# Optimization experiments

Measured on AMD Instinct MI355X. Metric: run time of the kernel, lower is better.

The kernel has to match this reference:

```python
import jax, jax.numpy as jnp
import numpy as np

B, M, D = 16384, 40, 32
INPUT_DIM = M * D  # 1280
CIN_SIZES = [128, 128]
DEEP_DIMS = [256, 128, 64]
EPS = 1e-5


def _init_linear(key, fan_in, fan_out):
    k1, k2 = jax.random.split(key)
    bound = 1.0 / np.sqrt(fan_in)
    w = jax.random.uniform(k1, (fan_out, fan_in), jnp.float32, -bound, bound)
    b = jax.random.uniform(k2, (fan_out,), jnp.float32, -bound, bound)
    return w, b


def setup_inputs() -> dict:
    key = jax.random.key(0)
    ks = jax.random.split(key, 12)
    x = jax.random.normal(ks[0], (B, INPUT_DIM), jnp.float32)
    emb_3d = jax.random.normal(ks[1], (B, M, D), jnp.float32)
    lin_w, lin_b = _init_linear(ks[2], INPUT_DIM, 1)
    # CIN conv1d (kernel_size=1) weights, flattened to [out, in]
    conv_w0, conv_b0 = _init_linear(ks[3], M * M, CIN_SIZES[0])          # in = 40*40
    prev1 = CIN_SIZES[0] // 2                                             # split_half
    conv_w1, conv_b1 = _init_linear(ks[4], M * prev1, CIN_SIZES[1])       # in = 40*64
    cin_out_dim = CIN_SIZES[0] // 2 + CIN_SIZES[1]                        # 192
    cin_out_w, cin_out_b = _init_linear(ks[5], cin_out_dim, 1)
    dims = [INPUT_DIM] + DEEP_DIMS
    deep_w0, deep_b0 = _init_linear(ks[6], dims[0], dims[1])
    deep_w1, deep_b1 = _init_linear(ks[7], dims[1], dims[2])
    deep_w2, deep_b2 = _init_linear(ks[8], dims[2], dims[3])
    ln_g0, ln_b0 = jnp.ones((dims[1],), jnp.float32), jnp.zeros((dims[1],), jnp.float32)
    ln_g1, ln_b1 = jnp.ones((dims[2],), jnp.float32), jnp.zeros((dims[2],), jnp.float32)
    ln_g2, ln_b2 = jnp.ones((dims[3],), jnp.float32), jnp.zeros((dims[3],), jnp.float32)
    return dict(x=x, emb_3d=emb_3d, lin_w=lin_w, lin_b=lin_b,
                conv_w0=conv_w0, conv_b0=conv_b0, conv_w1=conv_w1, conv_b1=conv_b1,
                cin_out_w=cin_out_w, cin_out_b=cin_out_b,
                deep_w0=deep_w0, deep_b0=deep_b0, ln_g0=ln_g0, ln_b0=ln_b0,
                deep_w1=deep_w1, deep_b1=deep_b1, ln_g1=ln_g1, ln_b1=ln_b1,
                deep_w2=deep_w2, deep_b2=deep_b2, ln_g2=ln_g2, ln_b2=ln_b2)


def _layernorm(h, g, b):
    mu = jnp.mean(h, axis=-1, keepdims=True)
    var = jnp.mean(jnp.square(h - mu), axis=-1, keepdims=True)
    return (h - mu) * jax.lax.rsqrt(var + EPS) * g + b


def _cin_layer(x0, xi, w, b):
    # outer = einsum('bmd,bnd->bmnd') then 1x1 conv over flattened (m*n).
    # Fused: contract the (m,n) outer product directly with the conv weight.
    o = w.shape[0]
    m, n = x0.shape[1], xi.shape[1]
    w3 = w.reshape(o, m, n)
    out = jnp.einsum('bmd,bnd,omn->bod', x0, xi, w3) + b[None, :, None]
    return jax.nn.relu(out)


def reference(x, emb_3d, lin_w, lin_b,
              conv_w0, conv_b0, conv_w1, conv_b1, cin_out_w, cin_out_b,
              deep_w0, deep_b0, ln_g0, ln_b0,
              deep_w1, deep_b1, ln_g1, ln_b1,
              deep_w2, deep_b2, ln_g2, ln_b2):
    aux = (x @ lin_w.T + lin_b)[:, 0]  # [B]

    # CIN with split_half=True
    x0 = emb_3d                                   # [B, 40, 32]
    out0 = _cin_layer(x0, x0, conv_w0, conv_b0)    # [B, 128, 32]
    h1, direct0 = jnp.split(out0, 2, axis=1)       # hidden gets FIRST half
    out1 = _cin_layer(x0, h1, conv_w1, conv_b1)    # [B, 128, 32]
    cin_feat = jnp.sum(jnp.concatenate([direct0, out1], axis=1), axis=2)  # [B, 192]
    aux = aux + (cin_feat @ cin_out_w.T + cin_out_b)[:, 0]

    # Deep tower (dropout = identity in eval)
    h = jax.nn.relu(_layernorm(x @ deep_w0.T + deep_b0, ln_g0, ln_b0))
    h = jax.nn.relu(_layernorm(h @ deep_w1.T + deep_b1, ln_g1, ln_b1))
    h = jax.nn.relu(_layernorm(h @ deep_w2.T + deep_b2, ln_g2, ln_b2))
    return h, aux
```

## Files before the change

### kernel.cpp

```cpp
#include <hip/hip_runtime.h>
#include <hip/hip_bf16.h>

typedef unsigned int u32;
typedef __attribute__((ext_vector_type(8))) short short8;
typedef __attribute__((ext_vector_type(8))) _Float16 half8;
typedef __attribute__((ext_vector_type(4))) float f32x4;

__device__ __forceinline__ u32 bf16_rne(float f) {
  u32 u = __builtin_bit_cast(u32, f);
  return (u + 0x7fffu + ((u >> 16) & 1u)) >> 16;
}
__device__ __forceinline__ u32 pk_bf16(float a, float b) {
  union { __hip_bfloat162 h; u32 u; } cv;
  cv.h = __float22bfloat162_rn(make_float2(a, b));
  return cv.u;
}
__device__ __forceinline__ unsigned short f16b(float f) {
  return __builtin_bit_cast(unsigned short, (_Float16)f);
}
__device__ __forceinline__ half8 splat8(_Float16 x) {
  return (half8){x, x, x, x, x, x, x, x};
}

__device__ __forceinline__ void glds16(const u32* g, u32* l) {
  __builtin_amdgcn_global_load_lds((const __attribute__((address_space(1))) u32*)g,
                                   (__attribute__((address_space(3))) u32*)l, 16, 0, 0);
}

__global__ void swz_kernel(const float* __restrict__ W, unsigned short* __restrict__ out,
                           int N, int K) {
  int tid = blockIdx.x * 256 + threadIdx.x;
  if (tid >= N * K) return;
  int j = tid & 7, l = (tid >> 3) & 63, rest = tid >> 9;
  int nt = N >> 4;
  int t = rest % nt, k32 = rest / nt;
  int o = t * 16 + (l & 15);
  int k = k32 * 32 + (l >> 4) * 8 + j;
  out[tid] = (unsigned short)bf16_rne(W[(size_t)o * K + k]);
}
__global__ void swz_f16_kernel(const float* __restrict__ W, unsigned short* __restrict__ out,
                               int N, int K) {
  int tid = blockIdx.x * 256 + threadIdx.x;
  if (tid >= N * K) return;
  int j = tid & 7, l = (tid >> 3) & 63, rest = tid >> 9;
  int nt = N >> 4;
  int t = rest % nt, k32 = rest / nt;
  int o = t * 16 + (l & 15);
  int k = k32 * 32 + (l >> 4) * 8 + j;
  out[tid] = f16b(W[(size_t)o * K + k]);
}

__global__ void tbl_kernel(u32* __restrict__ tbl0) {
  int g = threadIdx.x;
  if (g >= 120) return;
  int base = 0, m = 0;
  for (m = 0; m < 40; ++m) {
    int cnt = 5 - (m >> 3);
    if (g < base + cnt) break;
    base += cnt;
  }
  int n0 = 8 * ((m >> 3) + (g - base));
  tbl0[g] = (u32)m | ((u32)n0 << 8);
}

__global__ void swz0s_kernel(const float* __restrict__ W, const u32* __restrict__ tbl0,
                             unsigned short* __restrict__ out) {
  int tid = blockIdx.x * 256 + threadIdx.x;
  if (tid >= 960 * 128) return;
  int j = tid & 7, l = (tid >> 3) & 63, rest = tid >> 9;
  int t = rest & 7, k32 = rest >> 3;
  int o = t * 16 + (l & 15);
  int g = k32 * 4 + (l >> 4);
  u32 te = tbl0[g];
  int m = (int)(te & 255u), n0 = (int)(te >> 8);
  int n = n0 + j;
  float val;
  if (n < m) val = 0.f;
  else if (n == m) val = W[o * 1600 + m * 41];
  else val = W[o * 1600 + m * 40 + n] + W[o * 1600 + n * 40 + m];
  out[tid] = f16b(val);
}

__global__ void lin_kernel(const float* __restrict__ x, const float* __restrict__ lw,
                           const float* __restrict__ lb, const float* __restrict__ cb,
                           float* __restrict__ aux) {
  int row = blockIdx.x * 4 + (threadIdx.x >> 6);
  int lane = threadIdx.x & 63;
  const float4* xr = (const float4*)(x + (size_t)row * 1280);
  const float4* lw4 = (const float4*)lw;
  float s = 0.f;
#pragma unroll
  for (int e = 0; e < 5; ++e) {
    float4 a = xr[e * 64 + lane];
    float4 b = lw4[e * 64 + lane];
    s += a.x * b.x + a.y * b.y + a.z * b.z + a.w * b.w;
  }
#pragma unroll
  for (int m = 1; m < 64; m <<= 1) s += __shfl_xor(s, m, 64);
  if (lane == 0) aux[row] = s + lb[0] + cb[0];
}

__global__ __launch_bounds__(256, 2) void cin_kernel(
    const float* __restrict__ emb, const unsigned short* __restrict__ wz0s,
    const unsigned short* __restrict__ wz1, const u32* __restrict__ tbl0,
    const float* __restrict__ b0v, const float* __restrict__ b1v,
    const float* __restrict__ cw, float* __restrict__ aux) {
  __shared__ __align__(16) unsigned short Xh[128 * 40];
  __shared__ __align__(16) unsigned short h1s[128 * 72];
  __shared__ u32 tbl[120];
  __shared__ float auxacc[128];

  const int tid = threadIdx.x;
  const int lane = tid & 63;
  const int w = tid >> 6;
  const int wr = w >> 1, wc = w & 1;
  const int rl = lane & 15, q = lane >> 4;
  const int b0blk = blockIdx.x * 4;

#pragma unroll
  for (int i = 0; i < 5; ++i) {
    int idx = i * 256 + tid;
    int b = idx / 320;
    int rem = idx - b * 320;
    int m = rem >> 3, d0 = (rem & 7) * 4;
    float4 v = *(const float4*)(emb + ((size_t)(b0blk + b) * 40 + m) * 32 + d0);
    unsigned short* xc = &Xh[(b * 32 + d0) * 40 + m];
    xc[0] = f16b(v.x); xc[40] = f16b(v.y); xc[80] = f16b(v.z); xc[120] = f16b(v.w);
  }
  if (tid < 128) auxacc[tid] = 0.f;
  if (tid < 120) tbl[tid] = tbl0[tid];
  __syncthreads();

  f32x4 acc[4][4];
#pragma unroll
  for (int u = 0; u < 4; ++u)
#pragma unroll
    for (int t = 0; t < 4; ++t) acc[u][t] = f32x4{0.f, 0.f, 0.f, 0.f};

  {
    const u32* bptr = (const u32*)wz0s + wc * 1024 + lane * 4;
    const u32* xw = (const u32*)Xh;
    uint4 bA[4], bB[4];
    uint4 vnA[4], vnB[4];
    _Float16 xmA[4], xmB[4];

    auto loadB0 = [&](int kc, uint4* b) {
#pragma unroll
      for (int tt = 0; tt < 4; ++tt) b[tt] = *(const uint4*)(bptr + kc * 2048 + tt * 256);
    };
    auto loadA0 = [&](int kc, uint4* vn, _Float16* xm) {
      u32 te = tbl[kc * 4 + q];
      int mm = (int)(te & 255u);
      int w0 = (int)(te >> 8) >> 1;
#pragma unroll
      for (int u = 0; u < 4; ++u) {
        int r = 64 * wr + 16 * u + rl;
        vn[u] = *(const uint4*)(xw + r * 20 + w0);
        xm[u] = __builtin_bit_cast(_Float16, Xh[r * 40 + mm]);
      }
    };
    auto mfma0 = [&](const uint4* vn, const _Float16* xm, const uint4* bv) {
      __builtin_amdgcn_s_setprio(1);
#pragma unroll
      for (int u = 0; u < 4; ++u) {
        half8 af = __builtin_bit_cast(half8, vn[u]) * splat8(xm[u]);
#pragma unroll
        for (int tt = 0; tt < 4; ++tt)
          acc[u][tt] = __builtin_amdgcn_mfma_f32_16x16x32_f16(
              af, __builtin_bit_cast(half8, bv[tt]), acc[u][tt], 0, 0, 0);
      }
      __builtin_amdgcn_s_setprio(0);
    };

    loadB0(0, bA);
    loadA0(0, vnA, xmA);
    for (int kc = 0; kc < 30; kc += 2) {
      loadB0(kc + 1, bB);
      loadA0(kc + 1, vnB, xmB);
      mfma0(vnA, xmA, bA);
      int kn = (kc + 2 < 30) ? kc + 2 : 0;
      loadB0(kn, bA);
      loadA0(kn, vnA, xmA);
      mfma0(vnB, xmB, bB);
    }
  }

  if (wc == 0) {
#pragma unroll
    for (int u = 0; u < 4; ++u) {
      int r0q = 64 * wr + 16 * u + 4 * q;
#pragma unroll
      for (int tt = 0; tt < 4; ++tt) {
        int o = 16 * tt + rl;
        float bb = b0v[o];
#pragma unroll
        for (int i = 0; i < 4; ++i) {
          float vv = fmaxf(acc[u][tt][i] + bb, 0.f);
          h1s[(r0q + i) * 72 + o] = f16b(vv);
        }
      }
    }
  } else {
#pragma unroll
    for (int u = 0; u < 4; ++u)
#pragma unroll
      for (int i = 0; i < 4; ++i) {
        float sle = 0.f;
#pragma unroll
        for (int tt = 0; tt < 4; ++tt) {
          int o = 64 + 16 * tt + rl;
          sle += fmaxf(acc[u][tt][i] + b0v[o], 0.f) * cw[o - 64];
        }
        sle += __shfl_xor(sle, 1, 16);
        sle += __shfl_xor(sle, 2, 16);
        sle += __shfl_xor(sle, 4, 16);
        sle += __shfl_xor(sle, 8, 16);
        if (rl == 0) atomicAdd(&auxacc[64 * wr + 16 * u + 4 * q + i], sle);
      }
  }
#pragma unroll
  for (int u = 0; u < 4; ++u)
#pragma unroll
    for (int t = 0; t < 4; ++t) acc[u][t] = f32x4{0.f, 0.f, 0.f, 0.f};
  __syncthreads();

  {
    const u32* bptr = (const u32*)wz1 + wc * 1024 + lane * 4;
    const u32* hw = (const u32*)h1s;
    uint4 bA[4], bB[4];
    uint4 hpA[4], hpB[4];
    _Float16 xmA[4], xmB[4];

    auto loadB1 = [&](int kc, uint4* b) {
#pragma unroll
      for (int tt = 0; tt < 4; ++tt) b[tt] = *(const uint4*)(bptr + kc * 2048 + tt * 256);
    };
    auto loadH = [&](int kc, uint4* hp) {
      int wof = ((kc & 1) << 4) + 4 * q;
#pragma unroll
      for (int u = 0; u < 4; ++u) {
        int r = 64 * wr + 16 * u + rl;
        hp[u] = *(const uint4*)(hw + r * 36 + wof);
      }
    };
    auto loadXM = [&](int kp, _Float16* xm) {
#pragma unroll
      for (int u = 0; u < 4; ++u)
        xm[u] = __builtin_bit_cast(_Float16, Xh[(64 * wr + 16 * u + rl) * 40 + kp]);
    };
    auto mfma1 = [&](const uint4* hp, const _Float16* xm, const uint4* bv) {
      __builtin_amdgcn_s_setprio(1);
#pragma unroll
      for (int u = 0; u < 4; ++u) {
        half8 af = __builtin_bit_cast(half8, hp[u]) * splat8(xm[u]);
#pragma unroll
        for (int tt = 0; tt < 4; ++tt)
          acc[u][tt] = __builtin_amdgcn_mfma_f32_16x16x32_f16(
              af, __builtin_bit_cast(half8, bv[tt]), acc[u][tt], 0, 0, 0);
      }
      __builtin_amdgcn_s_setprio(0);
    };

    loadB1(0, bA);
    loadH(0, hpA);
    loadXM(0, xmA);
    for (int kp = 0; kp < 40; ++kp) {
      int kc = 2 * kp;
      loadB1(kc + 1, bB);
      loadH(kc + 1, hpB);
      mfma1(hpA, xmA, bA);
      int kc2 = (kc + 2 < 80) ? kc + 2 : 0;
      int kn = (kp + 1 < 40) ? kp + 1 : 0;
      loadB1(kc2, bA);
      loadH(kc2, hpA);
      loadXM(kn, xmB);
      mfma1(hpB, xmA, bB);
#pragma unroll
      for (int u = 0; u < 4; ++u) xmA[u] = xmB[u];
    }
  }

#pragma unroll
  for (int u = 0; u < 4; ++u)
#pragma unroll
    for (int i = 0; i < 4; ++i) {
      float sle = 0.f;
#pragma unroll
      for (int tt = 0; tt < 4; ++tt) {
        int o = 64 * wc + 16 * tt + rl;
        sle += fmaxf(acc[u][tt][i] + b1v[o], 0.f) * cw[64 + o];
      }
      sle += __shfl_xor(sle, 1, 16);
      sle += __shfl_xor(sle, 2, 16);
      sle += __shfl_xor(sle, 4, 16);
      sle += __shfl_xor(sle, 8, 16);
      if (rl == 0) atomicAdd(&auxacc[64 * wr + 16 * u + 4 * q + i], sle);
    }
  __syncthreads();
  if (tid < 4) {
    float ssum = 0.f;
    for (int d = 0; d < 32; ++d) ssum += auxacc[tid * 32 + d];
    aux[b0blk + tid] += ssum;
  }
}

template <int NT, bool AF32>
__global__ __launch_bounds__(256, 2) void gemm_deep(
    const void* __restrict__ Ain, const unsigned short* __restrict__ Bswz,
    const float* __restrict__ bias, float* __restrict__ Cout, int M, int N, int K) {
  __shared__ unsigned short At[128 * 40];
  __shared__ u32 Bt[NT * 256];
  const int tid = threadIdx.x, lane = tid & 63, w = tid >> 6;
  const int wr = w >> 1, wc = w & 1, rl = lane & 15, q = lane >> 4;
  const int r0 = blockIdx.x * 128, c0 = blockIdx.y * (NT * 16);
  const int ntg = N >> 4;
  constexpr int WT = NT / 2;
  f32x4 acc[4][WT];
#pragma unroll
  for (int u = 0; u < 4; ++u)
#pragma unroll
    for (int t = 0; t < WT; ++t) acc[u][t] = f32x4{0.f, 0.f, 0.f, 0.f};

  for (int kk = 0; kk < K; kk += 32) {
    __syncthreads();
    {
      int r = tid >> 1, kh = (tid & 1) * 16;
      if constexpr (AF32) {
        const float* A = (const float*)Ain;
        const float* src = A + (size_t)(r0 + r) * K + kk + kh;
        float4 v0 = *(const float4*)src;
        float4 v1 = *(const float4*)(src + 4);
        float4 v2 = *(const float4*)(src + 8);
        float4 v3 = *(const float4*)(src + 12);
        uint4 p0, p1;
        p0.x = pk_bf16(v0.x, v0.y); p0.y = pk_bf16(v0.z, v0.w);
        p0.z = pk_bf16(v1.x, v1.y); p0.w = pk_bf16(v1.z, v1.w);
        p1.x = pk_bf16(v2.x, v2.y); p1.y = pk_bf16(v2.z, v2.w);
        p1.z = pk_bf16(v3.x, v3.y); p1.w = pk_bf16(v3.z, v3.w);
        uint4* dst = (uint4*)&At[r * 40 + kh];
        dst[0] = p0;
        dst[1] = p1;
      } else {
        const unsigned short* A = (const unsigned short*)Ain;
        const uint4* src = (const uint4*)(A + (size_t)(r0 + r) * K + kk + kh);
        uint4* dst = (uint4*)&At[r * 40 + kh];
        dst[0] = src[0];
        dst[1] = src[1];
      }
      const u32* gb = (const u32*)Bswz + ((size_t)(kk >> 5) * ntg + (c0 >> 4)) * 256;
      constexpr int WW = NT * 64;
#pragma unroll
      for (int j = 0; j < NT / 4; ++j)
        glds16(gb + w * WW + j * 256 + lane * 4, &Bt[w * WW + j * 256]);
    }
    __syncthreads();
    short8 af[4];
#pragma unroll
    for (int u = 0; u < 4; ++u) {
      int rt = 4 * wr + u;
      uint4 av = *(const uint4*)&At[(16 * rt + rl) * 40 + q * 8];
      af[u] = __builtin_bit_cast(short8, av);
    }
#pragma unroll
    for (int tt = 0; tt < WT; ++tt) {
      int tg = WT * wc + tt;
      uint4 bv = *(const uint4*)&Bt[(tg * 64 + lane) * 4];
      short8 bfv = __builtin_bit_cast(short8, bv);
#pragma unroll
      for (int u = 0; u < 4; ++u)
        acc[u][tt] = __builtin_amdgcn_mfma_f32_16x16x32_bf16(af[u], bfv, acc[u][tt], 0, 0, 0);
    }
  }
#pragma unroll
  for (int u = 0; u < 4; ++u) {
    int rr = r0 + 64 * wr + 16 * u + 4 * q;
#pragma unroll
    for (int tt = 0; tt < WT; ++tt) {
      int o = c0 + (WT * wc + tt) * 16 + rl;
      float bb = bias[o];
#pragma unroll
      for (int i = 0; i < 4; ++i)
        Cout[(size_t)(rr + i) * N + o] = acc[u][tt][i] + bb;
    }
  }
}

template <int D, bool OUTF32>
__global__ void ln_relu_kernel(const float* __restrict__ in, const float* __restrict__ g,
                               const float* __restrict__ bt, void* __restrict__ out) {
  int row = blockIdx.x * 4 + (threadIdx.x >> 6);
  int lane = threadIdx.x & 63;
  constexpr int E = D / 64;
  const float* src = in + (size_t)row * D;
  float v[E], s1 = 0.f, s2 = 0.f;
#pragma unroll
  for (int e = 0; e < E; ++e) {
    v[e] = src[e * 64 + lane];
    s1 += v[e];
    s2 += v[e] * v[e];
  }
#pragma unroll
  for (int m = 1; m < 64; m <<= 1) {
    s1 += __shfl_xor(s1, m, 64);
    s2 += __shfl_xor(s2, m, 64);
  }
  float mu = s1 / (float)D;
  float rs = rsqrtf(s2 / (float)D - mu * mu + 1e-5f);
#pragma unroll
  for (int e = 0; e < E; ++e) {
    int c = e * 64 + lane;
    float y = fmaxf((v[e] - mu) * rs * g[c] + bt[c], 0.f);
    if constexpr (OUTF32)
      ((float*)out)[(size_t)row * D + c] = y;
    else
      ((unsigned short*)out)[(size_t)row * D + c] = (unsigned short)bf16_rne(y);
  }
}

extern "C" void kernel_launch(void* const* d_in, const int* in_sizes, int n_in,
                              void* d_out, int out_size, void* d_ws, size_t ws_size,
                              hipStream_t stream) {
  const float* x = (const float*)d_in[0];
  const float* emb = (const float*)d_in[1];
  const float* lin_w = (const float*)d_in[2];
  const float* lin_b = (const float*)d_in[3];
  const float* cw0 = (const float*)d_in[4];
  const float* cb0 = (const float*)d_in[5];
  const float* cw1 = (const float*)d_in[6];
  const float* cb1 = (const float*)d_in[7];
  const float* cow = (const float*)d_in[8];
  const float* cob = (const float*)d_in[9];
  const float* dw0 = (const float*)d_in[10];
  const float* db0 = (const float*)d_in[11];
  const float* g0 = (const float*)d_in[12];
  const float* be0 = (const float*)d_in[13];
  const float* dw1 = (const float*)d_in[14];
  const float* db1 = (const float*)d_in[15];
  const float* g1 = (const float*)d_in[16];
  const float* be1 = (const float*)d_in[17];
  const float* dw2 = (const float*)d_in[18];
  const float* db2 = (const float*)d_in[19];
  const float* g2 = (const float*)d_in[20];
  const float* be2 = (const float*)d_in[21];

  char* ws = (char*)d_ws;
  unsigned short* wz0s = (unsigned short*)(ws + 0);
  u32* tbl0 = (u32*)(ws + 245760);
  unsigned short* wz1 = (unsigned short*)(ws + 246272);
  unsigned short* wzd0 = (unsigned short*)(ws + 901632);
  unsigned short* wzd1 = (unsigned short*)(ws + 1556992);
  unsigned short* wzd2 = (unsigned short*)(ws + 1622528);
  float* t0 = (float*)(ws + 1638912);
  unsigned short* h0b = (unsigned short*)(ws + 18416128);
  float* t1 = (float*)(ws + 26804736);
  unsigned short* h1b = (unsigned short*)(ws + 35193344);
  float* t2 = (float*)(ws + 39387648);

  float* h_out = (float*)d_out;
  float* aux = h_out + (size_t)16384 * 64;

  tbl_kernel<<<1, 128, 0, stream>>>(tbl0);
  swz0s_kernel<<<480, 256, 0, stream>>>(cw0, tbl0, wz0s);
  swz_f16_kernel<<<(2560 * 128 + 255) / 256, 256, 0, stream>>>(cw1, wz1, 128, 2560);
  swz_kernel<<<(1280 * 256 + 255) / 256, 256, 0, stream>>>(dw0, wzd0, 256, 1280);
  swz_kernel<<<(256 * 128 + 255) / 256, 256, 0, stream>>>(dw1, wzd1, 128, 256);
  swz_kernel<<<(128 * 64 + 255) / 256, 256, 0, stream>>>(dw2, wzd2, 64, 128);

  lin_kernel<<<4096, 256, 0, stream>>>(x, lin_w, lin_b, cob, aux);
  cin_kernel<<<4096, 256, 0, stream>>>(emb, wz0s, wz1, tbl0, cb0, cb1, cow, aux);

  gemm_deep<8, true><<<dim3(128, 2), 256, 0, stream>>>(x, wzd0, db0, t0, 16384, 256, 1280);
  ln_relu_kernel<256, false><<<4096, 256, 0, stream>>>(t0, g0, be0, h0b);
  gemm_deep<8, false><<<dim3(128, 1), 256, 0, stream>>>(h0b, wzd1, db1, t1, 16384, 128, 256);
  ln_relu_kernel<128, false><<<4096, 256, 0, stream>>>(t1, g1, be1, h1b);
  gemm_deep<4, false><<<dim3(128, 1), 256, 0, stream>>>(h1b, wzd2, db2, t2, 16384, 64, 128);
  ln_relu_kernel<64, true><<<4096, 256, 0, stream>>>(t2, g2, be2, h_out);
}
```

Measured before the change: 627.1 us.

## Pad CIN LDS strides and halve deep GEMM row tile to 64

The CIN kernel's shared-memory row strides change (Xh 40→44 halfs, h1s 72→68 halfs) so that strided LDS reads and writes hit fewer bank conflicts. The deep-tower GEMM now uses 64-row tiles with all four waves split across columns instead of 128-row tiles in a 2x2 wave grid. That doubles the grid from 128 to 256 blocks so more of the GPU's compute units are busy. In exchange each B tile is reused across fewer rows, so more weight traffic goes to LDS, and each wave handles fewer column tiles.

```diff
diff --git a/kernel.cpp b/kernel.cpp
--- a/kernel.cpp
+++ b/kernel.cpp
@@ -105,8 +105,8 @@
     const unsigned short* __restrict__ wz1, const u32* __restrict__ tbl0,
     const float* __restrict__ b0v, const float* __restrict__ b1v,
     const float* __restrict__ cw, float* __restrict__ aux) {
-  __shared__ __align__(16) unsigned short Xh[128 * 40];
-  __shared__ __align__(16) unsigned short h1s[128 * 72];
+  __shared__ __align__(16) unsigned short Xh[128 * 44];
+  __shared__ __align__(16) unsigned short h1s[128 * 68];
   __shared__ u32 tbl[120];
   __shared__ float auxacc[128];
 
@@ -124,8 +124,8 @@
     int rem = idx - b * 320;
     int m = rem >> 3, d0 = (rem & 7) * 4;
     float4 v = *(const float4*)(emb + ((size_t)(b0blk + b) * 40 + m) * 32 + d0);
-    unsigned short* xc = &Xh[(b * 32 + d0) * 40 + m];
-    xc[0] = f16b(v.x); xc[40] = f16b(v.y); xc[80] = f16b(v.z); xc[120] = f16b(v.w);
+    unsigned short* xc = &Xh[(b * 32 + d0) * 44 + m];
+    xc[0] = f16b(v.x); xc[44] = f16b(v.y); xc[88] = f16b(v.z); xc[132] = f16b(v.w);
   }
   if (tid < 128) auxacc[tid] = 0.f;
   if (tid < 120) tbl[tid] = tbl0[tid];
@@ -155,8 +155,8 @@
 #pragma unroll
       for (int u = 0; u < 4; ++u) {
         int r = 64 * wr + 16 * u + rl;
-        vn[u] = *(const uint4*)(xw + r * 20 + w0);
-        xm[u] = __builtin_bit_cast(_Float16, Xh[r * 40 + mm]);
+        vn[u] = *(const uint4*)(xw + r * 22 + w0);
+        xm[u] = __builtin_bit_cast(_Float16, Xh[r * 44 + mm]);
       }
     };
     auto mfma0 = [&](const uint4* vn, const _Float16* xm, const uint4* bv) {
@@ -196,7 +196,7 @@
 #pragma unroll
         for (int i = 0; i < 4; ++i) {
           float vv = fmaxf(acc[u][tt][i] + bb, 0.f);
-          h1s[(r0q + i) * 72 + o] = f16b(vv);
+          h1s[(r0q + i) * 68 + o] = f16b(vv);
         }
       }
     }
@@ -240,13 +240,13 @@
 #pragma unroll
       for (int u = 0; u < 4; ++u) {
         int r = 64 * wr + 16 * u + rl;
-        hp[u] = *(const uint4*)(hw + r * 36 + wof);
+        hp[u] = *(const uint4*)(hw + r * 34 + wof);
       }
     };
     auto loadXM = [&](int kp, _Float16* xm) {
 #pragma unroll
       for (int u = 0; u < 4; ++u)
-        xm[u] = __builtin_bit_cast(_Float16, Xh[(64 * wr + 16 * u + rl) * 40 + kp]);
+        xm[u] = __builtin_bit_cast(_Float16, Xh[(64 * wr + 16 * u + rl) * 44 + kp]);
     };
     auto mfma1 = [&](const uint4* hp, const _Float16* xm, const uint4* bv) {
       __builtin_amdgcn_s_setprio(1);
@@ -305,16 +305,16 @@
 }
 
 template <int NT, bool AF32>
-__global__ __launch_bounds__(256, 2) void gemm_deep(
+__global__ __launch_bounds__(256, 2) void gemm_deep64(
     const void* __restrict__ Ain, const unsigned short* __restrict__ Bswz,
     const float* __restrict__ bias, float* __restrict__ Cout, int M, int N, int K) {
-  __shared__ unsigned short At[128 * 40];
+  __shared__ unsigned short At[64 * 40];
   __shared__ u32 Bt[NT * 256];
   const int tid = threadIdx.x, lane = tid & 63, w = tid >> 6;
-  const int wr = w >> 1, wc = w & 1, rl = lane & 15, q = lane >> 4;
-  const int r0 = blockIdx.x * 128, c0 = blockIdx.y * (NT * 16);
+  const int wc = w, rl = lane & 15, q = lane >> 4;
+  const int r0 = blockIdx.x * 64, c0 = blockIdx.y * (NT * 16);
   const int ntg = N >> 4;
-  constexpr int WT = NT / 2;
+  constexpr int WT = NT / 4;
   f32x4 acc[4][WT];
 #pragma unroll
   for (int u = 0; u < 4; ++u)
@@ -324,28 +324,19 @@
   for (int kk = 0; kk < K; kk += 32) {
     __syncthreads();
     {
-      int r = tid >> 1, kh = (tid & 1) * 16;
+      int r = tid >> 2, kh = (tid & 3) * 8;
       if constexpr (AF32) {
         const float* A = (const float*)Ain;
         const float* src = A + (size_t)(r0 + r) * K + kk + kh;
         float4 v0 = *(const float4*)src;
         float4 v1 = *(const float4*)(src + 4);
-        float4 v2 = *(const float4*)(src + 8);
-        float4 v3 = *(const float4*)(src + 12);
-        uint4 p0, p1;
+        uint4 p0;
         p0.x = pk_bf16(v0.x, v0.y); p0.y = pk_bf16(v0.z, v0.w);
         p0.z = pk_bf16(v1.x, v1.y); p0.w = pk_bf16(v1.z, v1.w);
-        p1.x = pk_bf16(v2.x, v2.y); p1.y = pk_bf16(v2.z, v2.w);
-        p1.z = pk_bf16(v3.x, v3.y); p1.w = pk_bf16(v3.z, v3.w);
-        uint4* dst = (uint4*)&At[r * 40 + kh];
-        dst[0] = p0;
-        dst[1] = p1;
+        *(uint4*)&At[r * 40 + kh] = p0;
       } else {
         const unsigned short* A = (const unsigned short*)Ain;
-        const uint4* src = (const uint4*)(A + (size_t)(r0 + r) * K + kk + kh);
-        uint4* dst = (uint4*)&At[r * 40 + kh];
-        dst[0] = src[0];
-        dst[1] = src[1];
+        *(uint4*)&At[r * 40 + kh] = *(const uint4*)(A + (size_t)(r0 + r) * K + kk + kh);
       }
       const u32* gb = (const u32*)Bswz + ((size_t)(kk >> 5) * ntg + (c0 >> 4)) * 256;
       constexpr int WW = NT * 64;
@@ -357,8 +348,7 @@
     short8 af[4];
 #pragma unroll
     for (int u = 0; u < 4; ++u) {
-      int rt = 4 * wr + u;
-      uint4 av = *(const uint4*)&At[(16 * rt + rl) * 40 + q * 8];
+      uint4 av = *(const uint4*)&At[(16 * u + rl) * 40 + q * 8];
       af[u] = __builtin_bit_cast(short8, av);
     }
 #pragma unroll
@@ -373,7 +363,7 @@
   }
 #pragma unroll
   for (int u = 0; u < 4; ++u) {
-    int rr = r0 + 64 * wr + 16 * u + 4 * q;
+    int rr = r0 + 16 * u + 4 * q;
 #pragma unroll
     for (int tt = 0; tt < WT; ++tt) {
       int o = c0 + (WT * wc + tt) * 16 + rl;
@@ -469,10 +459,10 @@
   lin_kernel<<<4096, 256, 0, stream>>>(x, lin_w, lin_b, cob, aux);
   cin_kernel<<<4096, 256, 0, stream>>>(emb, wz0s, wz1, tbl0, cb0, cb1, cow, aux);
 
-  gemm_deep<8, true><<<dim3(128, 2), 256, 0, stream>>>(x, wzd0, db0, t0, 16384, 256, 1280);
+  gemm_deep64<8, true><<<dim3(256, 2), 256, 0, stream>>>(x, wzd0, db0, t0, 16384, 256, 1280);
   ln_relu_kernel<256, false><<<4096, 256, 0, stream>>>(t0, g0, be0, h0b);
-  gemm_deep<8, false><<<dim3(128, 1), 256, 0, stream>>>(h0b, wzd1, db1, t1, 16384, 128, 256);
+  gemm_deep64<8, false><<<dim3(256, 1), 256, 0, stream>>>(h0b, wzd1, db1, t1, 16384, 128, 256);
   ln_relu_kernel<128, false><<<4096, 256, 0, stream>>>(t1, g1, be1, h1b);
-  gemm_deep<4, false><<<dim3(128, 1), 256, 0, stream>>>(h1b, wzd2, db2, t2, 16384, 64, 128);
+  gemm_deep64<4, false><<<dim3(256, 1), 256, 0, stream>>>(h1b, wzd2, db2, t2, 16384, 64, 128);
   ln_relu_kernel<64, true><<<4096, 256, 0, stream>>>(t2, g2, be2, h_out);
 }
```

New measurement: 705.7 us. +12.5%, slower.
